# Optimization experiments

Hardware: AMD Instinct MI355X
Metric: run time of the kernel (lower is better)

Reference implementation:

```python
import jax, jax.numpy as jnp
import numpy as np

B, S, H = 64, 512, 768
A1, C1 = 100, 300          # token-attention and sentence-classifier hidden sizes
BETA = 1.0                 # soft_attention_beta
SLW, TLW, RLW = 1.0, 1.0, 0.01  # loss weights


def setup_inputs() -> dict:
    key = jax.random.key(0)
    ks = jax.random.split(key, 12)
    hidden_states = jax.random.normal(ks[0], (B, S, H), jnp.float32)
    # token_attention: Linear(H,100) -> Tanh -> Linear(100,1) -> Sigmoid
    w1 = jax.random.normal(ks[1], (H, A1), jnp.float32) * 0.02
    b1 = jnp.zeros((A1,), jnp.float32)
    w2 = jax.random.normal(ks[2], (A1, 1), jnp.float32) * 0.02
    b2 = jnp.zeros((1,), jnp.float32)
    # sentence_classification: Linear(H,300) -> Tanh -> Linear(300,1) -> Sigmoid
    sw1 = jax.random.normal(ks[3], (H, C1), jnp.float32) * 0.02
    sb1 = jnp.zeros((C1,), jnp.float32)
    sw2 = jax.random.normal(ks[4], (C1, 1), jnp.float32) * 0.02
    sb2 = jnp.zeros((1,), jnp.float32)
    offset_mapping = jax.random.randint(ks[5], (B, S, 2), 0, 4).astype(jnp.int32)
    offset_mapping = offset_mapping.at[:, 0, 0].set(0)  # first token starts a word
    # labels in {-1, 0, 1}; -1 = ignore
    labels = jax.random.randint(ks[6], (B, S), -1, 2).astype(jnp.float32)
    return {
        "hidden_states": hidden_states,
        "w1": w1, "b1": b1, "w2": w2, "b2": b2,
        "sw1": sw1, "sb1": sb1, "sw2": sw2, "sb2": sb2,
        "labels": labels,
        "offset_mapping": offset_mapping,
    }


def _forward(hidden_states, w1, b1, w2, b2, sw1, sb1, sw2, sb2, labels, offset_mapping):
    # token attention scores in (0,1): [B, S]
    token_att = jax.nn.sigmoid(
        jnp.tanh(hidden_states @ w1 + b1) @ w2 + b2
    )[..., 0]

    # ragged per-word subword max-pooling (segment-max along the sequence)
    not_subword = offset_mapping[:, :, 0] == 0                 # [B, S] word starts
    seg = jnp.maximum(jnp.cumsum(not_subword.astype(jnp.int32), axis=1) - 1, 0)

    def _seg_max(vals, seg_ids):
        return jax.ops.segment_max(vals, seg_ids, num_segments=S)

    segmax = jax.vmap(_seg_max)(token_att, seg)                # [B, S] per-word max
    word_att = jnp.where(not_subword, jnp.take_along_axis(segmax, seg, axis=1), 0.0)

    # mask: labeled tokens that are word starts
    token_mask = ((labels != -1) & not_subword).astype(token_att.dtype)
    masked = word_att * token_mask                              # token_logits [B, S]

    # beta-normalized soft attention pooling over hidden states
    p = masked ** BETA
    att_norm = p / jnp.sum(p, axis=1, keepdims=True)            # [B, S]
    pooled = jnp.einsum("bsh,bs->bh", hidden_states, att_norm)  # [B, H]

    sent = jax.nn.sigmoid(jnp.tanh(pooled @ sw1 + sb1) @ sw2 + sb2)  # [B, 1]

    # losses (MSE with reduction='sum')
    sentence_labels = jnp.max(labels, axis=1, keepdims=True)    # [B, 1]
    sentence_loss = jnp.sum((sent - sentence_labels) ** 2)
    zero_labels = jnp.where(labels != -1, labels, 0.0)
    token_loss = jnp.sum((masked - zero_labels) ** 2)
    ones_masked = jnp.where(masked == 0, 1.0, masked)
    reg_a = jnp.sum(jnp.min(ones_masked, axis=1, keepdims=True) ** 2)
    reg_b = jnp.sum((jnp.max(masked, axis=1, keepdims=True) - sentence_labels) ** 2)
    total = SLW * sentence_loss + TLW * token_loss + RLW * (reg_a + reg_b)
    return total, sentence_loss, token_loss, reg_a, reg_b, masked, sent


def reference(hidden_states, w1, b1, w2, b2, sw1, sb1, sw2, sb2, labels, offset_mapping):
    return _forward(hidden_states, w1, b1, w2, b2, sw1, sb1, sw2, sb2,
                    labels, offset_mapping)
```

## Files before the change

### kernel.cpp

```cpp
#include <hip/hip_runtime.h>
#include <math.h>

#define BB 64
#define SS 512
#define HH 768
#define AA1 100
#define CC1 300

typedef __bf16 bf16x8 __attribute__((ext_vector_type(8)));
typedef float f32x4 __attribute__((ext_vector_type(4)));

__global__ __launch_bounds__(256) void k_prep(const float* __restrict__ w1,
                                              __bf16* __restrict__ w1i) {
    int idx = blockIdx.x * 256 + threadIdx.x;
    int j = idx % 112;
    int r = idx / 112;
    int e = r & 7, g = r >> 3;
    int k = (g >> 2) * 32 + (g & 3) * 8 + e;
    float v = (j < AA1) ? w1[k * AA1 + j] : 0.f;
    w1i[((size_t)g * 112 + j) * 8 + e] = (__bf16)v;
}

__global__ __launch_bounds__(256) void k_token_att(
        const float* __restrict__ hs, const __bf16* __restrict__ w1i,
        const float* __restrict__ b1, const float* __restrict__ w2,
        const float* __restrict__ b2, float* __restrict__ token_att) {
    const int tid = threadIdx.x;
    const int tok0 = blockIdx.x * 64;
    const int w = tid >> 6, lane = tid & 63;
    const int q = lane >> 4, ln = lane & 15;
    const int trow = tok0 + w * 16 + ln;

    f32x4 acc[7];
#pragma unroll
    for (int n = 0; n < 7; n++) acc[n] = (f32x4){0.f, 0.f, 0.f, 0.f};

    const float* ga = hs + (size_t)trow * HH + q * 8;
    const __bf16* gb = w1i + (size_t)(q * 112 + ln) * 8;

#pragma unroll 4
    for (int kt = 0; kt < 24; kt++) {
        f32x4 a0 = *(const f32x4*)(ga + kt * 32);
        f32x4 a1 = *(const f32x4*)(ga + kt * 32 + 4);
        bf16x8 af;
#pragma unroll
        for (int e = 0; e < 4; e++) {
            af[e] = (__bf16)a0[e];
            af[e + 4] = (__bf16)a1[e];
        }
        const __bf16* gbk = gb + (size_t)kt * 3584;
#pragma unroll
        for (int n = 0; n < 7; n++) {
            bf16x8 bf = *(const bf16x8*)(gbk + n * 128);
            acc[n] = __builtin_amdgcn_mfma_f32_16x16x32_bf16(af, bf, acc[n], 0, 0, 0);
        }
    }

    float s0 = 0.f, s1 = 0.f, s2 = 0.f, s3 = 0.f;
#pragma unroll
    for (int n = 0; n < 7; n++) {
        int j = n * 16 + ln;
        if (j < AA1) {
            float bj = b1[j], wj = w2[j];
            s0 += tanhf(acc[n][0] + bj) * wj;
            s1 += tanhf(acc[n][1] + bj) * wj;
            s2 += tanhf(acc[n][2] + bj) * wj;
            s3 += tanhf(acc[n][3] + bj) * wj;
        }
    }
#pragma unroll
    for (int off = 1; off < 16; off <<= 1) {
        s0 += __shfl_xor(s0, off); s1 += __shfl_xor(s1, off);
        s2 += __shfl_xor(s2, off); s3 += __shfl_xor(s3, off);
    }
    if (ln == 0) {
        float bb = b2[0];
        int base = tok0 + w * 16 + q * 4;
        token_att[base + 0] = 1.f / (1.f + expf(-(s0 + bb)));
        token_att[base + 1] = 1.f / (1.f + expf(-(s1 + bb)));
        token_att[base + 2] = 1.f / (1.f + expf(-(s2 + bb)));
        token_att[base + 3] = 1.f / (1.f + expf(-(s3 + bb)));
    }
}

__global__ __launch_bounds__(256) void k_poolmask(
        const float* __restrict__ hs, const float* __restrict__ token_att,
        const float* __restrict__ labels, const int* __restrict__ offm,
        float* __restrict__ masked_out, float* __restrict__ pooled,
        float4* __restrict__ stats_g, float* __restrict__ zsum,
        int* __restrict__ cnt2) {
    __shared__ int smax[SS];
    __shared__ float wl[SS];
    __shared__ short il[SS];
    __shared__ float red[256];
    __shared__ int wscan[4];
    __shared__ int wscan2[4];
    __shared__ float wred[5][4];
    __shared__ float sh_inv;
    __shared__ int sh_nnz;

    const int b = blockIdx.x, hc = blockIdx.y;
    const int t = threadIdx.x;
    const int lane = t & 63, wv = t >> 6;
    const int s0 = 2 * t, s1 = s0 + 1;

    const int4 om = ((const int4*)offm)[b * 256 + t];
    const int ns0 = (om.x == 0) ? 1 : 0;
    const int ns1 = (om.z == 0) ? 1 : 0;

    int v = ns0 + ns1;
#pragma unroll
    for (int off = 1; off < 64; off <<= 1) {
        int o = __shfl_up(v, off);
        if (lane >= off) v += o;
    }
    if (lane == 63) wscan[wv] = v;
    smax[s0] = 0;
    smax[s1] = 0;
    __syncthreads();
    int woff = 0;
    for (int i = 0; i < 4; i++) woff += (i < wv) ? wscan[i] : 0;
    const int cum1 = v + woff;
    const int cum0 = cum1 - ns1;
    const int seg0 = max(cum0 - 1, 0);
    const int seg1 = max(cum1 - 1, 0);

    const float2 ta = ((const float2*)token_att)[b * 256 + t];
    atomicMax(&smax[seg0], __float_as_int(ta.x));
    atomicMax(&smax[seg1], __float_as_int(ta.y));
    __syncthreads();

    const float2 lab = ((const float2*)labels)[b * 256 + t];
    const float wa0 = ns0 ? __int_as_float(smax[seg0]) : 0.f;
    const float wa1 = ns1 ? __int_as_float(smax[seg1]) : 0.f;
    const float m0 = (lab.x != -1.f && ns0) ? wa0 : 0.f;
    const float m1 = (lab.y != -1.f && ns1) ? wa1 : 0.f;
    if (hc == 0) {
        masked_out[b * SS + s0] = m0;
        masked_out[b * SS + s1] = m1;
    }
    const float zl0 = (lab.x != -1.f) ? lab.x : 0.f;
    const float zl1 = (lab.y != -1.f) ? lab.y : 0.f;
    const float tl0 = (m0 - zl0) * (m0 - zl0);
    const float tl1 = (m1 - zl1) * (m1 - zl1);
    const float on0 = (m0 == 0.f) ? 1.f : m0;
    const float on1 = (m1 == 0.f) ? 1.f : m1;

    float r0 = m0 + m1, r1 = tl0 + tl1;
    float r2 = fmaxf(m0, m1), r3 = fminf(on0, on1), r4 = fmaxf(lab.x, lab.y);
#pragma unroll
    for (int off = 32; off > 0; off >>= 1) {
        r0 += __shfl_xor(r0, off);
        r1 += __shfl_xor(r1, off);
        r2 = fmaxf(r2, __shfl_xor(r2, off));
        r3 = fminf(r3, __shfl_xor(r3, off));
        r4 = fmaxf(r4, __shfl_xor(r4, off));
    }
    if (lane == 0) {
        wred[0][wv] = r0; wred[1][wv] = r1; wred[2][wv] = r2;
        wred[3][wv] = r3; wred[4][wv] = r4;
    }

    const int nz0 = (m0 != 0.f) ? 1 : 0;
    const int nz1 = (m1 != 0.f) ? 1 : 0;
    int v2 = nz0 + nz1;
#pragma unroll
    for (int off = 1; off < 64; off <<= 1) {
        int o = __shfl_up(v2, off);
        if (lane >= off) v2 += o;
    }
    if (lane == 63) wscan2[wv] = v2;
    __syncthreads();
    int woff2 = 0;
    for (int i = 0; i < 4; i++) woff2 += (i < wv) ? wscan2[i] : 0;
    const int incl = v2 + woff2;
    if (nz1) { wl[incl - 1] = m1; il[incl - 1] = (short)s1; }
    if (nz0) { wl[incl - 1 - nz1] = m0; il[incl - 1 - nz1] = (short)s0; }

    if (t == 0) {
        float att = 0.f, tokl = 0.f, maxm = -1e30f, minone = 1e30f, slab = -1e30f;
        int nz = 0;
        for (int i = 0; i < 4; i++) {
            att += wred[0][i]; tokl += wred[1][i];
            maxm = fmaxf(maxm, wred[2][i]);
            minone = fminf(minone, wred[3][i]);
            slab = fmaxf(slab, wred[4][i]);
            nz += wscan2[i];
        }
        sh_inv = 1.f / att;
        sh_nnz = nz;
        if (hc == 0) {
            stats_g[b] = make_float4(tokl, maxm, minone, slab);
            zsum[b] = 0.f;
            if (b == 0) *cnt2 = 0;
        }
    }
    __syncthreads();

    const int nnz = sh_nnz;
    const float inv = sh_inv;
    const int h = (t & 63) + hc * 64;
    const int slot = t >> 6;
    const float* hsb = hs + (size_t)b * SS * HH + h;
    const int len = (nnz + 3) >> 2;
    const int i0 = slot * len;
    const int i1 = min(i0 + len, nnz);
    float a0 = 0.f, a1 = 0.f, a2 = 0.f, a3 = 0.f;
    int i = i0;
    for (; i + 4 <= i1; i += 4) {
        a0 += hsb[(size_t)il[i]     * HH] * wl[i];
        a1 += hsb[(size_t)il[i + 1] * HH] * wl[i + 1];
        a2 += hsb[(size_t)il[i + 2] * HH] * wl[i + 2];
        a3 += hsb[(size_t)il[i + 3] * HH] * wl[i + 3];
    }
    for (; i < i1; i++) a0 += hsb[(size_t)il[i] * HH] * wl[i];
    red[t] = (a0 + a1) + (a2 + a3);
    __syncthreads();
    if (t < 64)
        pooled[(size_t)b * HH + h] =
            (red[t] + red[t + 64] + red[t + 128] + red[t + 192]) * inv;
}

__global__ __launch_bounds__(256) void k_sentloss(
        const float* __restrict__ pooled, const float* __restrict__ sw1,
        const float* __restrict__ sb1, const float* __restrict__ sw2,
        const float* __restrict__ sb2, const float4* __restrict__ stats_g,
        float* __restrict__ zsum, int* __restrict__ cnt2,
        float* __restrict__ sent_out, float* __restrict__ out) {
    __shared__ float pl[HH];
    __shared__ float red[256];
    __shared__ int lastF;

    const int b = blockIdx.x, cc = blockIdx.y;
    const int tid = threadIdx.x;
    pl[tid]       = pooled[(size_t)b * HH + tid];
    pl[tid + 256] = pooled[(size_t)b * HH + tid + 256];
    pl[tid + 512] = pooled[(size_t)b * HH + tid + 512];
    __syncthreads();

    const int cl = tid & 63, kq = tid >> 6;
    const int c = cc * 60 + cl;
    float z = 0.f;
    if (cl < 60) {
        const int k0 = kq * 192;
        for (int k = k0; k < k0 + 192; k += 8) {
#pragma unroll
            for (int u = 0; u < 8; u++)
                z += pl[k + u] * sw1[(size_t)(k + u) * CC1 + c];
        }
    }
    red[tid] = z;
    __syncthreads();
    if (kq == 0) {
        float zz = red[tid] + red[tid + 64] + red[tid + 128] + red[tid + 192];
        float tt = 0.f;
        if (cl < 60) tt = tanhf(zz + sb1[c]) * sw2[c];
#pragma unroll
        for (int off = 32; off > 0; off >>= 1) tt += __shfl_xor(tt, off);
        if (cl == 0) atomicAdd(&zsum[b], tt);
    }
    __syncthreads();

    if (tid == 0) {
        __threadfence();
        int old = atomicAdd(cnt2, 1);
        lastF = (old == BB * 5 - 1) ? 1 : 0;
    }
    __syncthreads();
    if (!lastF) return;
    __threadfence();

    if (tid < 64) {
        const float zs = atomicAdd(&zsum[tid], 0.f);
        const float sv = 1.f / (1.f + expf(-(zs + sb2[0])));
        sent_out[tid] = sv;
        const float4 st = stats_g[tid];
        float vs = sv - st.w; vs *= vs;
        float ra = st.z * st.z;
        float rb = st.y - st.w; rb *= rb;
        float s0 = vs, s1 = st.x, s2 = ra, s3 = rb;
#pragma unroll
        for (int off = 32; off > 0; off >>= 1) {
            s0 += __shfl_xor(s0, off);
            s1 += __shfl_xor(s1, off);
            s2 += __shfl_xor(s2, off);
            s3 += __shfl_xor(s3, off);
        }
        if (tid == 0) {
            out[1] = s0; out[2] = s1; out[3] = s2; out[4] = s3;
            out[0] = s0 + s1 + 0.01f * (s2 + s3);
        }
    }
}

extern "C" void kernel_launch(void* const* d_in, const int* in_sizes, int n_in,
                              void* d_out, int out_size, void* d_ws, size_t ws_size,
                              hipStream_t stream) {
    const float* hs  = (const float*)d_in[0];
    const float* w1  = (const float*)d_in[1];
    const float* b1  = (const float*)d_in[2];
    const float* w2  = (const float*)d_in[3];
    const float* b2  = (const float*)d_in[4];
    const float* sw1 = (const float*)d_in[5];
    const float* sb1 = (const float*)d_in[6];
    const float* sw2 = (const float*)d_in[7];
    const float* sb2 = (const float*)d_in[8];
    const float* labels = (const float*)d_in[9];
    const int*   offm   = (const int*)d_in[10];

    float* out = (float*)d_out;
    float* ws  = (float*)d_ws;

    float*  token_att = ws;
    __bf16* w1i    = (__bf16*)(ws + 32768);
    float*  pooled = ws + 75776;
    float*  zsum   = ws + 124928;
    float4* stats  = (float4*)(ws + 124992);
    int*    cnt2   = (int*)(ws + 125248);

    float* masked_out = out + 5;
    float* sent_out   = out + 5 + BB * SS;

    hipLaunchKernelGGL(k_prep, dim3(336), dim3(256), 0, stream, w1, w1i);
    hipLaunchKernelGGL(k_token_att, dim3(512), dim3(256), 0, stream,
                       hs, w1i, b1, w2, b2, token_att);
    hipLaunchKernelGGL(k_poolmask, dim3(BB, 12), dim3(256), 0, stream,
                       hs, token_att, labels, offm, masked_out,
                       pooled, stats, zsum, cnt2);
    hipLaunchKernelGGL(k_sentloss, dim3(BB, 5), dim3(256), 0, stream,
                       pooled, sw1, sb1, sw2, sb2, stats, zsum, cnt2,
                       sent_out, out);
}
```

Before: 209.8 us.

## Transpose sentence-classifier weights for vectorized dot products and widen pooling grid

The prep kernel now also transposes sw1 into a workspace buffer, when the workspace is large enough, so the sentence classifier can read contiguous float4 rows instead of strided columns. Separately, the pooling kernel's grid doubles from 12 to 24 column chunks of 32 hidden units, with 8 sequence slots per block instead of 4, to raise parallelism on the gather-weighted sum. The costs are an extra transpose pass over sw1 and more blocks that each redo the per-batch mask and statistics prologue.

After: 208.8 us. Within noise of the previous version (-0.5%).

```diff
diff --git a/kernel.cpp b/kernel.cpp
--- a/kernel.cpp
+++ b/kernel.cpp
@@ -11,14 +11,24 @@
 typedef float f32x4 __attribute__((ext_vector_type(4)));
 
 __global__ __launch_bounds__(256) void k_prep(const float* __restrict__ w1,
-                                              __bf16* __restrict__ w1i) {
-    int idx = blockIdx.x * 256 + threadIdx.x;
-    int j = idx % 112;
-    int r = idx / 112;
-    int e = r & 7, g = r >> 3;
-    int k = (g >> 2) * 32 + (g & 3) * 8 + e;
-    float v = (j < AA1) ? w1[k * AA1 + j] : 0.f;
-    w1i[((size_t)g * 112 + j) * 8 + e] = (__bf16)v;
+                                              __bf16* __restrict__ w1i,
+                                              const float* __restrict__ sw1,
+                                              float* __restrict__ sw1T,
+                                              int doT) {
+    const int bb = blockIdx.x;
+    if (bb < 336) {
+        int idx = bb * 256 + threadIdx.x;
+        int j = idx % 112;
+        int r = idx / 112;
+        int e = r & 7, g = r >> 3;
+        int k = (g >> 2) * 32 + (g & 3) * 8 + e;
+        float v = (j < AA1) ? w1[k * AA1 + j] : 0.f;
+        w1i[((size_t)g * 112 + j) * 8 + e] = (__bf16)v;
+    } else if (doT) {
+        int idx = (bb - 336) * 256 + threadIdx.x;
+        int k = idx / CC1, c = idx - k * CC1;
+        sw1T[(size_t)c * HH + k] = sw1[idx];
+    }
 }
 
 __global__ __launch_bounds__(256) void k_token_att(
@@ -199,10 +209,10 @@
 
     const int nnz = sh_nnz;
     const float inv = sh_inv;
-    const int h = (t & 63) + hc * 64;
-    const int slot = t >> 6;
+    const int h = (t & 31) + hc * 32;
+    const int slot = t >> 5;
     const float* hsb = hs + (size_t)b * SS * HH + h;
-    const int len = (nnz + 3) >> 2;
+    const int len = (nnz + 7) >> 3;
     const int i0 = slot * len;
     const int i1 = min(i0 + len, nnz);
     float a0 = 0.f, a1 = 0.f, a2 = 0.f, a3 = 0.f;
@@ -216,18 +226,22 @@
     for (; i < i1; i++) a0 += hsb[(size_t)il[i] * HH] * wl[i];
     red[t] = (a0 + a1) + (a2 + a3);
     __syncthreads();
-    if (t < 64)
-        pooled[(size_t)b * HH + h] =
-            (red[t] + red[t + 64] + red[t + 128] + red[t + 192]) * inv;
+    if (t < 32) {
+        float p = 0.f;
+#pragma unroll
+        for (int sl = 0; sl < 8; sl++) p += red[t + sl * 32];
+        pooled[(size_t)b * HH + h] = p * inv;
+    }
 }
 
 __global__ __launch_bounds__(256) void k_sentloss(
         const float* __restrict__ pooled, const float* __restrict__ sw1,
-        const float* __restrict__ sb1, const float* __restrict__ sw2,
-        const float* __restrict__ sb2, const float4* __restrict__ stats_g,
-        float* __restrict__ zsum, int* __restrict__ cnt2,
-        float* __restrict__ sent_out, float* __restrict__ out) {
-    __shared__ float pl[HH];
+        const float* __restrict__ sw1T, const float* __restrict__ sb1,
+        const float* __restrict__ sw2, const float* __restrict__ sb2,
+        const float4* __restrict__ stats_g, float* __restrict__ zsum,
+        int* __restrict__ cnt2, float* __restrict__ sent_out,
+        float* __restrict__ out, int useT) {
+    __shared__ __attribute__((aligned(16))) float pl[HH];
     __shared__ float red[256];
     __shared__ int lastF;
 
@@ -242,11 +256,21 @@
     const int c = cc * 60 + cl;
     float z = 0.f;
     if (cl < 60) {
-        const int k0 = kq * 192;
-        for (int k = k0; k < k0 + 192; k += 8) {
-#pragma unroll
-            for (int u = 0; u < 8; u++)
-                z += pl[k + u] * sw1[(size_t)(k + u) * CC1 + c];
+        if (useT) {
+            const float4* wp = (const float4*)(sw1T + (size_t)c * HH + kq * 192);
+            const float4* pp = (const float4*)(pl + kq * 192);
+#pragma unroll 8
+            for (int u = 0; u < 48; u++) {
+                float4 a = pp[u], w4 = wp[u];
+                z += a.x * w4.x + a.y * w4.y + a.z * w4.z + a.w * w4.w;
+            }
+        } else {
+            const int k0 = kq * 192;
+            for (int k = k0; k < k0 + 192; k += 8) {
+#pragma unroll
+                for (int u = 0; u < 8; u++)
+                    z += pl[k + u] * sw1[(size_t)(k + u) * CC1 + c];
+            }
         }
     }
     red[tid] = z;
@@ -317,17 +341,21 @@
     float*  zsum   = ws + 124928;
     float4* stats  = (float4*)(ws + 124992);
     int*    cnt2   = (int*)(ws + 125248);
+    float*  sw1T   = ws + 131072;
+
+    const int doT = (ws_size >= (size_t)(131072 + 230400) * sizeof(float)) ? 1 : 0;
 
     float* masked_out = out + 5;
     float* sent_out   = out + 5 + BB * SS;
 
-    hipLaunchKernelGGL(k_prep, dim3(336), dim3(256), 0, stream, w1, w1i);
+    hipLaunchKernelGGL(k_prep, dim3(doT ? 1236 : 336), dim3(256), 0, stream,
+                       w1, w1i, sw1, sw1T, doT);
     hipLaunchKernelGGL(k_token_att, dim3(512), dim3(256), 0, stream,
                        hs, w1i, b1, w2, b2, token_att);
-    hipLaunchKernelGGL(k_poolmask, dim3(BB, 12), dim3(256), 0, stream,
+    hipLaunchKernelGGL(k_poolmask, dim3(BB, 24), dim3(256), 0, stream,
                        hs, token_att, labels, offm, masked_out,
                        pooled, stats, zsum, cnt2);
     hipLaunchKernelGGL(k_sentloss, dim3(BB, 5), dim3(256), 0, stream,
-                       pooled, sw1, sb1, sw2, sb2, stats, zsum, cnt2,
-                       sent_out, out);
-}
+                       pooled, sw1, sw1T, sb1, sw2, sb2, stats, zsum, cnt2,
+                       sent_out, out, doT);
+}
```
